# Optimization experiments

Hardware: AMD Instinct MI355X
Metric: run time of the kernel (lower is better)

The kernel has to match this reference:

```python
import jax, jax.numpy as jnp
import numpy as np

N_QUBITS = 14
Q_DEPTH = 4
N_GEN = 8
BATCH = 512

# CNOT in (control, target) basis ordering |00,01,10,11>
_CNOT = jnp.array([[1., 0., 0., 0.],
                   [0., 1., 0., 0.],
                   [0., 0., 0., 1.],
                   [0., 0., 1., 0.]], dtype=jnp.float32)


def _ry(t):
    c = jnp.cos(t / 2)
    s = jnp.sin(t / 2)
    return jnp.stack([jnp.stack([c, -s]), jnp.stack([s, c])])  # [2,2]


def _apply_1q(state, gate, w):
    # state: (2,)*n real tensor; apply 2x2 gate on wire w
    n = state.ndim
    st = jnp.moveaxis(state, w, 0).reshape(2, -1)
    st = gate @ st
    return jnp.moveaxis(st.reshape((2,) * n), 0, w)


def _apply_2q(state, gate, w0, w1):
    n = state.ndim
    st = jnp.moveaxis(state, (w0, w1), (0, 1)).reshape(4, -1)
    st = gate @ st
    return jnp.moveaxis(st.reshape((2,) * n), (0, 1), (w0, w1))


def _circuit(theta):
    # EfficientSU2-with-circular-entanglement circuit, repeated Q_DEPTH times.
    # RY + CNOT on |0...0> keeps amplitudes real -> float32 statevector.
    state = jnp.zeros((2,) * N_QUBITS, dtype=jnp.float32).at[(0,) * N_QUBITS].set(1.0)
    for _ in range(Q_DEPTH):
        for i in range(N_QUBITS):
            state = _apply_1q(state, _ry(theta[i]), i)
        for i in range(N_QUBITS):
            state = _apply_2q(state, _CNOT, i, (i + 1) % N_QUBITS)
        for i in range(N_QUBITS):
            state = _apply_1q(state, _ry(theta[i]), i)
    probs = state * state
    # <Z_i> = P(bit_i = 0) - P(bit_i = 1)
    z = []
    for i in range(N_QUBITS):
        p = jnp.moveaxis(probs, i, 0).reshape(2, -1).sum(axis=1)
        z.append(p[0] - p[1])
    return jnp.stack(z)  # [n_qubits]


def setup_inputs() -> dict:
    key = jax.random.key(0)
    k1, k2, k3 = jax.random.split(key, 3)
    x = jax.random.normal(k1, (BATCH, N_QUBITS), dtype=jnp.float32)
    # q_params: per-generator n_qubits x n_qubits matrices (orthogonal-ish small init)
    W = jax.random.normal(k2, (N_GEN, N_QUBITS, N_QUBITS), dtype=jnp.float32) * 0.01
    b = jax.random.uniform(k3, (N_GEN, N_QUBITS), minval=-0.01, maxval=0.01, dtype=jnp.float32)
    return {"x": x, "W": W, "b": b}


def reference(x, W, b):
    # theta[b,g] = x[b] @ W[g] + b[g]   -> [B, G, n_qubits]
    theta = jnp.einsum('bq,gqp->bgp', x, W) + b[None]
    expvals = jax.vmap(jax.vmap(_circuit))(theta)  # [B, G, n_qubits]
    return expvals.reshape(x.shape[0], -1)  # [B, G*n_qubits]
```

## Files before the change

kernel.cpp:

```cpp
#include <hip/hip_runtime.h>
#include <hip/hip_fp16.h>
#include <stdint.h>

#define NQ 14
#define NPASS 5
#define NGEN 8
#define NTH 256
#define NBLK (512*NGEN)

typedef float f2 __attribute__((ext_vector_type(2)));

constexpr int cpop16(uint32_t x){ int n=0; for(int i=0;i<16;++i) n+=(x>>i)&1; return n; }

struct Mat { uint16_t col[NQ]; };
struct Tables {
    uint16_t mask[NPASS][NQ];
    uint16_t rho [NPASS][NQ];
    uint16_t zrho[NQ];
    bool ok;
};
constexpr uint16_t ring_apply(uint16_t j) {
    for (int i = 0; i < NQ; ++i) { int t=(i+1)%NQ; j=(uint16_t)(j ^ (((j>>i)&1u)<<t)); }
    return j;
}
constexpr Mat identity() { Mat m{}; for (int i=0;i<NQ;++i) m.col[i]=(uint16_t)(1u<<i); return m; }
constexpr uint16_t mat_row(const Mat& L, int r) {
    uint16_t v=0; for (int b=0;b<NQ;++b) v=(uint16_t)(v | (((L.col[b]>>r)&1u)<<b)); return v;
}
constexpr uint16_t mat_apply(const Mat& L, uint16_t x) {
    uint16_t r=0; for (int b=0;b<NQ;++b) if ((x>>b)&1u) r=(uint16_t)(r ^ L.col[b]); return r;
}
constexpr Mat inverse(const Mat& L, bool& ok) {
    uint32_t lrow[NQ]={}, irow[NQ]={};
    for (int r=0;r<NQ;++r){ lrow[r]=mat_row(L,r); irow[r]=1u<<r; }
    for (int c=0;c<NQ;++c){
        int piv=-1;
        for (int r=c;r<NQ;++r) if ((lrow[r]>>c)&1u){ piv=r; break; }
        if (piv<0){ ok=false; return identity(); }
        uint32_t tl=lrow[c]; lrow[c]=lrow[piv]; lrow[piv]=tl;
        uint32_t ti=irow[c]; irow[c]=irow[piv]; irow[piv]=ti;
        for (int r=0;r<NQ;++r) if (r!=c && ((lrow[r]>>c)&1u)){ lrow[r]^=lrow[c]; irow[r]^=irow[c]; }
    }
    Mat inv{};
    for (int w=0;w<NQ;++w){ uint16_t cv=0; for (int r=0;r<NQ;++r) cv=(uint16_t)(cv | (((irow[r]>>w)&1u)<<r)); inv.col[w]=cv; }
    return inv;
}
constexpr Mat mat_mul(const Mat& A, const Mat& B) {
    Mat r{}; for (int j=0;j<NQ;++j) r.col[j]=mat_apply(A,B.col[j]); return r;
}
constexpr uint16_t mat_tapply(const Mat& M, uint16_t r) {
    uint16_t v=0; for (int j=0;j<NQ;++j) v=(uint16_t)(v | ((uint16_t)(cpop16(M.col[j]&r)&1)<<j)); return v;
}
constexpr Tables build() {
    Tables t{}; t.ok = true;
    Mat L = identity();
    for (int p=0;p<NPASS;++p) {
        if (p>0) { Mat Ln{}; for (int b=0;b<NQ;++b) Ln.col[b]=ring_apply(L.col[b]); L=Ln; }
        bool ok = true; Mat inv = inverse(L, ok); if (!ok) t.ok = false;
        for (int w=0;w<NQ;++w) {
            t.mask[p][w] = inv.col[w];
            t.rho [p][w] = mat_row(L,w);
            if (mat_apply(L, inv.col[w]) != (uint16_t)(1u<<w)) t.ok = false;
        }
    }
    for (int w=0;w<NQ;++w) t.zrho[w] = mat_row(L,w);
    return t;
}
constexpr Tables TBL = build();
static_assert(TBL.ok, "GF2 table build failed");
static_assert(TBL.mask[0][0]==1 && TBL.rho[0][0]==1, "pass0 w0");
static_assert(TBL.mask[1][0]==3,      "pass1 w0 mask");
static_assert(TBL.rho [1][0]==0x3FFE, "pass1 w0 rho");
static_assert(TBL.mask[1][12]==0x3000,"pass1 w12 mask");

#define MAXPH 28
#define MAXG 14
struct Sched {
    bool ok; int nph; int ngtot;
    uint16_t M[MAXPH][NQ];
    int ng[MAXPH];
    int gw[MAXPH][MAXG]; int gsc[MAXPH][MAXG];
    uint16_t gmu[MAXPH][MAXG];
    uint16_t grho[MAXPH][MAXG];
    uint16_t zrho[NQ];
};
struct Basis { uint16_t lead[16]; };
constexpr bool binsert(Basis& B, uint16_t v) {
    v &= 0x3FFC;
    while (v) {
        int t=-1; for (int i=15;i>=0;--i) if ((v>>i)&1u){ t=i; break; }
        if (!B.lead[t]) { B.lead[t]=v; return true; }
        v = (uint16_t)(v ^ B.lead[t]);
    }
    return false;
}
constexpr Sched try_build(int u0,int u1,int u2) {
    Sched S{}; S.ok=true; S.nph=0; S.ngtot=0;
    const uint16_t lam[3] = { (uint16_t)((1u<<2)|(1u<<u0)), (uint16_t)((1u<<3)|(1u<<u1)), (uint16_t)((1u<<4)|(1u<<u2)) };
    Mat prevT = identity();
    bool done[NPASS][NQ] = {};
    int pend[NPASS] = {};
    for (int p=1;p<NPASS;++p) pend[p]=NQ;
    int pc = 1; int guard = 0;
    while (pc < NPASS) {
        if (pend[pc]==0) { ++pc; continue; }
        if (S.nph>=MAXPH || ++guard>MAXPH){ S.ok=false; return S; }
        const int ph = S.nph++;
        Basis B{};
        if(!binsert(B,lam[0])||!binsert(B,lam[1])||!binsert(B,lam[2])){ S.ok=false; return S; }
        Mat T{}; T.col[0]=1; T.col[1]=2; T.col[2]=lam[0]; T.col[3]=lam[1]; T.col[4]=lam[2];
        int nsl=0;
        for (int round=0;round<2 && nsl<4;++round)
            for (int w=0;w<NQ && nsl<4;++w) {
                if (done[pc][w]) continue;
                const uint16_t m=TBL.mask[pc][w];
                if ((m & ~3u)==0) continue;
                const bool stuck = ((m & 0x3FE0u)==0);
                if ((round==0)!=stuck) continue;
                if (binsert(B,(uint16_t)(m&~3u))) T.col[10+nsl++]=(uint16_t)(m&~3u);
            }
        int freecols[9]; int nf=0;
        for (int c=5;c<=9;++c)        freecols[nf++]=c;
        for (int c=10+nsl;c<=13;++c)  freecols[nf++]=c;
        int filled=0;
        for (int b=5;b<NQ && filled<nf;++b) if (binsert(B,(uint16_t)(1u<<b))) T.col[freecols[filled++]]=(uint16_t)(1u<<b);
        for (int b=2;b<5  && filled<nf;++b) if (binsert(B,(uint16_t)(1u<<b))) T.col[freecols[filled++]]=(uint16_t)(1u<<b);
        if (filled!=nf){ S.ok=false; return S; }
        bool iok=true; const Mat Ti=inverse(T,iok); if(!iok){ S.ok=false; return S; }
        S.ng[ph]=0;
        for (int w=0;w<NQ;++w) {
            if (done[pc][w]) continue;
            const uint16_t mu=mat_apply(Ti,TBL.mask[pc][w]);
            if (mu & 0x03FCu) continue;
            const int gi=S.ng[ph]++; ++S.ngtot;
            S.gw[ph][gi]=w; S.gsc[ph][gi]=(pc==NPASS-1)?0:1;
            S.gmu[ph][gi]=(uint16_t)(((mu>>10)<<2)|(mu&3u));
            S.grho[ph][gi]=mat_tapply(T,TBL.rho[pc][w]);
            done[pc][w]=true; --pend[pc];
        }
        if (S.ng[ph]==0){ S.ok=false; return S; }
        if (pend[pc]==0 && pc+1<NPASS) {
            const int p2=pc+1;
            for (int w=0;w<NQ;++w) {
                if (done[p2][w]) continue;
                const uint16_t mu=mat_apply(Ti,TBL.mask[p2][w]);
                if (mu & 0x03FCu) continue;
                const int gi=S.ng[ph]++; ++S.ngtot;
                S.gw[ph][gi]=w; S.gsc[ph][gi]=(p2==NPASS-1)?0:1;
                S.gmu[ph][gi]=(uint16_t)(((mu>>10)<<2)|(mu&3u));
                S.grho[ph][gi]=mat_tapply(T,TBL.rho[p2][w]);
                done[p2][w]=true; --pend[p2];
            }
        }
        bool iok2=true; const Mat Pi=inverse(prevT,iok2); if(!iok2){ S.ok=false; return S; }
        const Mat M=mat_mul(Pi,T);
        if (M.col[0]!=1u || M.col[1]!=2u){ S.ok=false; return S; }
        for (int c=2;c<NQ;++c) if (M.col[c]&3u){ S.ok=false; return S; }
        for (int c=2;c<5;++c)  if ((M.col[c]&0x1Cu)!=(1u<<c)){ S.ok=false; return S; }
        for (int c=0;c<NQ;++c) S.M[ph][c]=M.col[c];
        prevT=T;
    }
    for (int w=0;w<NQ;++w) S.zrho[w]=mat_tapply(prevT,TBL.zrho[w]);
    return S;
}
constexpr Sched build_sched() {
    Sched S = try_build(5,6,7);    if (S.ok) return S;
    S = try_build(8,9,10);         if (S.ok) return S;
    S = try_build(11,12,13);       if (S.ok) return S;
    S = try_build(5,9,13);         if (S.ok) return S;
    S = try_build(13,9,5);         if (S.ok) return S;
    S = try_build(6,7,8);          if (S.ok) return S;
    S = try_build(9,10,11);        if (S.ok) return S;
    S = try_build(7,5,6);          return S;
}
constexpr Sched SCH = build_sched();
static_assert(SCH.ok, "frame schedule build failed");
static_assert(SCH.ngtot == 4*NQ, "not all 56 gates scheduled");
constexpr int NPH = SCH.nph;
static_assert(NPH >= 5 && NPH <= MAXPH, "unexpected phase count");

struct __align__(8) H4 { __half2 lo, hi; };
static __device__ __forceinline__ H4 pk4(f2 a, f2 b) {
    H4 r; r.lo = __floats2half2_rn(a.x, a.y); r.hi = __floats2half2_rn(b.x, b.y); return r;
}
static __device__ __forceinline__ f2 unpk_lo(const H4& h) {
    float2 f = __half22float2(h.lo); return f2{f.x, f.y};
}
static __device__ __forceinline__ f2 unpk_hi(const H4& h) {
    float2 f = __half22float2(h.hi); return f2{f.x, f.y};
}

template<int PH> __device__ __forceinline__
void run_phase(f2 (&qq)[32], unsigned tid, H4* Aq, const float (&CS)[2][2][NQ]) {
    unsigned tq = 0;
    #pragma unroll
    for (int k=0;k<8;++k) {
        const unsigned col = ((unsigned)SCH.M[PH][2+k]) >> 2;
        tq ^= (((tid>>k)&1u) ? col : 0u);
    }
    #pragma unroll
    for (int IT=0;IT<16;++IT) {
        unsigned cit = 0;
        if (IT&1) cit ^= ((unsigned)SCH.M[PH][10])>>2;
        if (IT&2) cit ^= ((unsigned)SCH.M[PH][11])>>2;
        if (IT&4) cit ^= ((unsigned)SCH.M[PH][12])>>2;
        if (IT&8) cit ^= ((unsigned)SCH.M[PH][13])>>2;
        const H4 v = Aq[tq ^ cit];
        qq[2*IT]   = unpk_lo(v);
        qq[2*IT+1] = unpk_hi(v);
    }
    #pragma unroll
    for (int gi=0; gi<SCH.ng[PH]; ++gi) {
        const int w = SCH.gw[PH][gi], sc = SCH.gsc[PH][gi];
        const unsigned lm  = SCH.gmu[PH][gi];
        const unsigned rho = SCH.grho[PH][gi];
        const float cc = CS[sc][0][w], sv = CS[sc][1][w];
        const unsigned pt = __popc(rho & (tid<<2)) & 1u;
        const float u  = pt ? sv : -sv;
        const f2 c2 = {cc, cc};
        const f2 uu = {u, u};
        const f2 un = {u, -u};
        const unsigned di = ((lm>>1)&1u) | ((lm>>2)<<1);
        if (di == 0u) {
            #pragma unroll
            for (int i=0;i<32;++i) {
                const unsigned ya0 = ((unsigned)(i&1)<<1) | (((unsigned)i>>1)<<10);
                const int s0 = __popc(rho & ya0) & 1;
                const int s1 = __popc(rho & (ya0|1u)) & 1;
                const f2 a = qq[i];
                const f2 pv = __builtin_shufflevector(a, a, 1, 0);
                const f2 t = (s0==s1) ? uu : un;
                qq[i] = __builtin_elementwise_fma(s0 ? -t : t, pv, c2*a);
            }
        } else {
            const int dpiv = 1 << (31 - __builtin_clz(di));
            const int jsw = (int)(lm & 1u);
            #pragma unroll
            for (int i=0;i<32;++i) {
                if (i & dpiv) continue;
                const int i2 = i ^ (int)di;
                const unsigned ya0 = ((unsigned)(i &1)<<1) | (((unsigned)i >>1)<<10);
                const unsigned yb0 = ((unsigned)(i2&1)<<1) | (((unsigned)i2>>1)<<10);
                const int sa0 = __popc(rho & ya0)&1,      sa1 = __popc(rho & (ya0|1u))&1;
                const int sb0 = __popc(rho & yb0)&1,      sb1 = __popc(rho & (yb0|1u))&1;
                const f2 a = qq[i], b = qq[i2];
                const f2 pa = jsw ? __builtin_shufflevector(b,b,1,0) : b;
                const f2 pb = jsw ? __builtin_shufflevector(a,a,1,0) : a;
                const f2 ta = (sa0==sa1) ? uu : un;
                const f2 tb = (sb0==sb1) ? uu : un;
                qq[i]  = __builtin_elementwise_fma(sa0 ? -ta : ta, pa, c2*a);
                qq[i2] = __builtin_elementwise_fma(sb0 ? -tb : tb, pb, c2*b);
            }
        }
    }
}

template<int PH> __device__ __forceinline__
void phases_from(f2 (&qq)[32], unsigned tid, H4* Aq, const float (&CS)[2][2][NQ]) {
    if constexpr (PH < NPH) {
        run_phase<PH>(qq, tid, Aq, CS);
        if constexpr (PH+1 < NPH) {
            __syncthreads();
            #pragma unroll
            for (int IT=0;IT<16;++IT)
                Aq[((unsigned)IT<<8)|tid] = pk4(qq[2*IT], qq[2*IT+1]);
            __syncthreads();
        }
        phases_from<PH+1>(qq, tid, Aq, CS);
    }
}

__global__ __launch_bounds__(NTH)
void qgen_kernel(const float* __restrict__ x, const float* __restrict__ W,
                 const float* __restrict__ bias, float* __restrict__ out)
{
    __shared__ H4 Aq[4096];
    __shared__ float CS[2][2][NQ];
    __shared__ float zacc[NQ];

    const int blk = blockIdx.x;
    const int bb  = blk >> 3;
    const int g   = blk & 7;
    const unsigned tid = threadIdx.x;

    if (tid < NQ) {
        float acc = bias[g*NQ + tid];
        #pragma unroll
        for (int qq2=0;qq2<NQ;++qq2) acc += x[bb*NQ+qq2] * W[(g*NQ+qq2)*NQ + tid];
        float h = 0.5f*acc;
        CS[0][0][tid]=cosf(h);   CS[0][1][tid]=sinf(h);
        CS[1][0][tid]=cosf(acc); CS[1][1][tid]=sinf(acc);
        zacc[tid]=0.f;
    }
    __syncthreads();

    f2 qq[32];
    {
        float tp = 1.f;
        #pragma unroll
        for (int k=0;k<8;++k) tp *= ((tid>>k)&1u) ? CS[0][1][2+k] : CS[0][0][2+k];
        const float c0=CS[0][0][0], s0=CS[0][1][0], c1=CS[0][0][1], s1=CS[0][1][1];
        #pragma unroll
        for (int IT=0;IT<16;++IT) {
            float f = tp;
            #pragma unroll
            for (int b=0;b<4;++b) f *= ((IT>>b)&1) ? CS[0][1][10+b] : CS[0][0][10+b];
            qq[2*IT]   = f2{f*c0*c1, f*s0*c1};
            qq[2*IT+1] = f2{f*c0*s1, f*s0*s1};
        }
        #pragma unroll
        for (int IT=0;IT<16;++IT)
            Aq[((unsigned)IT<<8)|tid] = pk4(qq[2*IT], qq[2*IT+1]);
        __syncthreads();
    }

    phases_from<0>(qq, tid, Aq, CS);

    f2 h[32];
    #pragma unroll
    for (int i=0;i<32;++i) h[i] = qq[i]*qq[i];
    #pragma unroll
    for (int b=0;b<5;++b) {
        #pragma unroll
        for (int i=0;i<32;++i) {
            if (i & (1<<b)) continue;
            const int i2 = i | (1<<b);
            const f2 xv = h[i], yv = h[i2];
            h[i] = xv + yv; h[i2] = xv - yv;
        }
    }
    #pragma unroll
    for (int w=0;w<NQ;++w) {
        const unsigned zr = SCH.zrho[w];
        const int ri = (int)(((zr>>1)&1u) | (((zr>>10)&0xFu)<<1));
        float val = (zr&1u) ? (h[ri].x - h[ri].y) : (h[ri].x + h[ri].y);
        if (__popc(zr & (tid<<2)) & 1) val = -val;
        #pragma unroll
        for (int off=32; off; off>>=1) val += __shfl_down(val, off, 64);
        if ((tid & 63u) == 0) atomicAdd(&zacc[w], val);
    }
    __syncthreads();
    if (tid < NQ) out[blk*NQ + tid] = zacc[tid];
}

extern "C" void kernel_launch(void* const* d_in, const int* in_sizes, int n_in,
                              void* d_out, int out_size, void* d_ws, size_t ws_size,
                              hipStream_t stream) {
    (void)in_sizes; (void)n_in; (void)d_ws; (void)ws_size; (void)out_size;
    const float* x    = (const float*)d_in[0];
    const float* W    = (const float*)d_in[1];
    const float* bias = (const float*)d_in[2];
    float* out = (float*)d_out;
    qgen_kernel<<<dim3(NBLK), dim3(NTH), 0, stream>>>(x, W, bias, out);
}
```

Measured before the change: 258.1 us.

## Swizzle shared-memory statevector layout and use packed-FMA inline asm for rotations

Adds an XOR swizzle (q ^ q>>4 ^ q>>8) to every shared-memory address of the half-precision statevector, on both the store and the permuted gather. The aim is to cut LDS bank conflicts in the gathers between phases. It also replaces the compiler-generated vector FMA with inline v_pk_mul_f32/v_pk_fma_f32 asm, using op_sel to do the lane swap inside the instruction and precomputed sign vectors. Inline asm can stop the compiler from scheduling around these instructions, and the swizzle must be linear over XOR to stay correct.

```diff
diff --git a/kernel.cpp b/kernel.cpp
--- a/kernel.cpp
+++ b/kernel.cpp
@@ -11,6 +11,8 @@
 typedef float f2 __attribute__((ext_vector_type(2)));
 
 constexpr int cpop16(uint32_t x){ int n=0; for(int i=0;i<16;++i) n+=(x>>i)&1; return n; }
+
+__host__ __device__ constexpr unsigned swz(unsigned q){ return q ^ (q>>4) ^ (q>>8); }
 
 struct Mat { uint16_t col[NQ]; };
 struct Tables {
@@ -190,6 +192,17 @@
     float2 f = __half22float2(h.hi); return f2{f.x, f.y};
 }
 
+static __device__ __forceinline__ f2 pk_mul(f2 a, f2 b) {
+    f2 d; asm("v_pk_mul_f32 %0, %1, %2" : "=v"(d) : "v"(a), "v"(b)); return d;
+}
+static __device__ __forceinline__ f2 pk_fma(f2 a, f2 b, f2 c) {
+    f2 d; asm("v_pk_fma_f32 %0, %1, %2, %3" : "=v"(d) : "v"(a), "v"(b), "v"(c)); return d;
+}
+static __device__ __forceinline__ f2 pk_fma_swap1(f2 a, f2 b, f2 c) {
+    f2 d; asm("v_pk_fma_f32 %0, %1, %2, %3 op_sel:[0,1,0] op_sel_hi:[1,0,1]"
+              : "=v"(d) : "v"(a), "v"(b), "v"(c)); return d;
+}
+
 template<int PH> __device__ __forceinline__
 void run_phase(f2 (&qq)[32], unsigned tid, H4* Aq, const float (&CS)[2][2][NQ]) {
     unsigned tq = 0;
@@ -198,6 +211,7 @@
         const unsigned col = ((unsigned)SCH.M[PH][2+k]) >> 2;
         tq ^= (((tid>>k)&1u) ? col : 0u);
     }
+    const unsigned stq = swz(tq);
     #pragma unroll
     for (int IT=0;IT<16;++IT) {
         unsigned cit = 0;
@@ -205,7 +219,7 @@
         if (IT&2) cit ^= ((unsigned)SCH.M[PH][11])>>2;
         if (IT&4) cit ^= ((unsigned)SCH.M[PH][12])>>2;
         if (IT&8) cit ^= ((unsigned)SCH.M[PH][13])>>2;
-        const H4 v = Aq[tq ^ cit];
+        const H4 v = Aq[stq ^ swz(cit)];
         qq[2*IT]   = unpk_lo(v);
         qq[2*IT+1] = unpk_hi(v);
     }
@@ -217,24 +231,25 @@
         const float cc = CS[sc][0][w], sv = CS[sc][1][w];
         const unsigned pt = __popc(rho & (tid<<2)) & 1u;
         const float u  = pt ? sv : -sv;
-        const f2 c2 = {cc, cc};
-        const f2 uu = {u, u};
-        const f2 un = {u, -u};
+        const f2 c2  = {cc, cc};
+        const f2 p00 = { u,  u};
+        const f2 p01 = { u, -u};
+        const f2 p10 = {-u,  u};
+        const f2 p11 = {-u, -u};
         const unsigned di = ((lm>>1)&1u) | ((lm>>2)<<1);
+        const int jsw = (int)(lm & 1u);
         if (di == 0u) {
             #pragma unroll
             for (int i=0;i<32;++i) {
                 const unsigned ya0 = ((unsigned)(i&1)<<1) | (((unsigned)i>>1)<<10);
                 const int s0 = __popc(rho & ya0) & 1;
                 const int s1 = __popc(rho & (ya0|1u)) & 1;
-                const f2 a = qq[i];
-                const f2 pv = __builtin_shufflevector(a, a, 1, 0);
-                const f2 t = (s0==s1) ? uu : un;
-                qq[i] = __builtin_elementwise_fma(s0 ? -t : t, pv, c2*a);
+                const f2 sp = s0 ? (s1 ? p11 : p10) : (s1 ? p01 : p00);
+                const f2 t = pk_mul(c2, qq[i]);
+                qq[i] = pk_fma_swap1(sp, qq[i], t);
             }
         } else {
             const int dpiv = 1 << (31 - __builtin_clz(di));
-            const int jsw = (int)(lm & 1u);
             #pragma unroll
             for (int i=0;i<32;++i) {
                 if (i & dpiv) continue;
@@ -243,13 +258,18 @@
                 const unsigned yb0 = ((unsigned)(i2&1)<<1) | (((unsigned)i2>>1)<<10);
                 const int sa0 = __popc(rho & ya0)&1,      sa1 = __popc(rho & (ya0|1u))&1;
                 const int sb0 = __popc(rho & yb0)&1,      sb1 = __popc(rho & (yb0|1u))&1;
+                const f2 spA = sa0 ? (sa1 ? p11 : p10) : (sa1 ? p01 : p00);
+                const f2 spB = sb0 ? (sb1 ? p11 : p10) : (sb1 ? p01 : p00);
                 const f2 a = qq[i], b = qq[i2];
-                const f2 pa = jsw ? __builtin_shufflevector(b,b,1,0) : b;
-                const f2 pb = jsw ? __builtin_shufflevector(a,a,1,0) : a;
-                const f2 ta = (sa0==sa1) ? uu : un;
-                const f2 tb = (sb0==sb1) ? uu : un;
-                qq[i]  = __builtin_elementwise_fma(sa0 ? -ta : ta, pa, c2*a);
-                qq[i2] = __builtin_elementwise_fma(sb0 ? -tb : tb, pb, c2*b);
+                const f2 ta = pk_mul(c2, a);
+                const f2 tb = pk_mul(c2, b);
+                if (jsw) {
+                    qq[i]  = pk_fma_swap1(spA, b, ta);
+                    qq[i2] = pk_fma_swap1(spB, a, tb);
+                } else {
+                    qq[i]  = pk_fma(spA, b, ta);
+                    qq[i2] = pk_fma(spB, a, tb);
+                }
             }
         }
     }
@@ -261,9 +281,10 @@
         run_phase<PH>(qq, tid, Aq, CS);
         if constexpr (PH+1 < NPH) {
             __syncthreads();
+            const unsigned stid = swz(tid);
             #pragma unroll
             for (int IT=0;IT<16;++IT)
-                Aq[((unsigned)IT<<8)|tid] = pk4(qq[2*IT], qq[2*IT+1]);
+                Aq[swz((unsigned)IT<<8) ^ stid] = pk4(qq[2*IT], qq[2*IT+1]);
             __syncthreads();
         }
         phases_from<PH+1>(qq, tid, Aq, CS);
@@ -308,9 +329,10 @@
             qq[2*IT]   = f2{f*c0*c1, f*s0*c1};
             qq[2*IT+1] = f2{f*c0*s1, f*s0*s1};
         }
+        const unsigned stid = swz(tid);
         #pragma unroll
         for (int IT=0;IT<16;++IT)
-            Aq[((unsigned)IT<<8)|tid] = pk4(qq[2*IT], qq[2*IT+1]);
+            Aq[swz((unsigned)IT<<8) ^ stid] = pk4(qq[2*IT], qq[2*IT+1]);
         __syncthreads();
     }
 
```

Result: slower. 275.2 us (+6.6%).
